# Optimization experiments

Hardware: AMD Instinct MI355X
Metric: run time of the kernel (lower is better)

Reference implementation:

```python
import jax, jax.numpy as jnp
import numpy as np
import math

DIM = 768
HEADS = 8
DIM_HEAD = 64
INNER = HEADS * DIM_HEAD  # 512
B, L = 2, 4096
LN_EPS = 1e-5


def setup_inputs() -> dict:
    key = jax.random.key(0)
    ks = jax.random.split(key, 6)
    std = 0.02
    return {
        "x": jax.random.normal(ks[0], (B, L, DIM), dtype=jnp.float32),
        "ln_gamma": jnp.ones((DIM,), dtype=jnp.float32),
        "ln_beta": jnp.zeros((DIM,), dtype=jnp.float32),
        "Wq": jax.random.normal(ks[1], (DIM, INNER), dtype=jnp.float32) * std,
        "Wkv": jax.random.normal(ks[2], (DIM, 2 * INNER), dtype=jnp.float32) * std,
        "Wo": jax.random.normal(ks[3], (INNER, DIM), dtype=jnp.float32) * std,
    }


def reference(x, ln_gamma, ln_beta, Wq, Wkv, Wo):
    b, l, _ = x.shape
    # LayerNorm (eps=1e-5, affine)
    mu = jnp.mean(x, axis=-1, keepdims=True)
    var = jnp.mean(jnp.square(x - mu), axis=-1, keepdims=True)
    xn = (x - mu) * jax.lax.rsqrt(var + LN_EPS) * ln_gamma + ln_beta

    q = xn @ Wq                      # (b, l, inner)
    kv = xn @ Wkv                    # (b, l, 2*inner)
    k, v = jnp.split(kv, 2, axis=-1)

    def to_heads(t):
        return t.reshape(b, l, HEADS, DIM_HEAD).transpose(0, 2, 1, 3)  # (b,h,l,d)

    q, k, v = to_heads(q), to_heads(k), to_heads(v)

    scale = 1.0 / math.sqrt(math.sqrt(DIM_HEAD))
    # explicit quadratic scores, softmax in float32 as in original
    weight = jnp.einsum("bhid,bhjd->bhij", q * scale, k * scale)
    weight = jax.nn.softmax(weight.astype(jnp.float32), axis=-1).astype(q.dtype)
    out = jnp.einsum("bhij,bhjd->bhid", weight, v)       # (b,h,l,d)
    out = out.transpose(0, 2, 1, 3).reshape(b, l, INNER)  # merge heads
    return out @ Wo
```

## Files before the change

kernel.cpp:

```cpp
#include <hip/hip_runtime.h>
#include <hip/hip_bf16.h>


typedef __bf16 bf16_t;
typedef __bf16 bf16x4 __attribute__((ext_vector_type(4)));
typedef __bf16 bf16x8 __attribute__((ext_vector_type(8)));
typedef float f32x4 __attribute__((ext_vector_type(4)));
typedef float f32x16 __attribute__((ext_vector_type(16)));
typedef unsigned int u32x2 __attribute__((ext_vector_type(2)));
typedef unsigned int u32x4 __attribute__((ext_vector_type(4)));

#define MFMA16(a, b, c) __builtin_amdgcn_mfma_f32_16x16x32_bf16((a), (b), (c), 0, 0, 0)
#define MFMA32(a, b, c) __builtin_amdgcn_mfma_f32_32x32x16_bf16((a), (b), (c), 0, 0, 0)

#define QSCALE 0.18033688011112042f

#define GLDS(gp, lp)                                                          \
    __builtin_amdgcn_global_load_lds(                                         \
        (const __attribute__((address_space(1))) void*)(gp),                  \
        (__attribute__((address_space(3))) void*)(lp), 16, 0, 0)

__device__ __forceinline__ int detect_f32(const unsigned int* __restrict__ xw) {
    const int l = threadIdx.x & 63;
    int cnt = 0;
#pragma unroll
    for (int j = 0; j < 2; ++j) {
        const unsigned int e = (xw[l * 2 + j] >> 7) & 0xFF;
        cnt += (e >= 100 && e <= 140) ? 1 : 0;
    }
#pragma unroll
    for (int off = 1; off < 64; off <<= 1) cnt += __shfl_xor(cnt, off, 64);
    return cnt < 64;
}

__global__ __launch_bounds__(256) void prep_kernel(
    const void* __restrict__ xv, const void* __restrict__ gv,
    const void* __restrict__ bv, const void* __restrict__ wq,
    const void* __restrict__ wkv, const void* __restrict__ wo,
    bf16_t* __restrict__ xn, bf16_t* __restrict__ WqkvT, bf16_t* __restrict__ WoT,
    int* __restrict__ flag) {
    const int f32 = detect_f32((const unsigned int*)xv);
    const int bid = blockIdx.x;
    const int t = threadIdx.x;
    if (bid == 0 && t == 0) *flag = f32;

    __shared__ bf16_t Ts[64 * 68];

    if (bid < 2048) {
        const int lane = t & 63;
        const int row = bid * 4 + (t >> 6);
        const int c0 = lane * 12;
        float v[12];
        if (f32) {
            const float* xr = (const float*)xv + (size_t)row * 768 + c0;
#pragma unroll
            for (int i = 0; i < 3; ++i) {
                const float4 q = *(const float4*)(xr + i * 4);
                v[i * 4] = q.x; v[i * 4 + 1] = q.y;
                v[i * 4 + 2] = q.z; v[i * 4 + 3] = q.w;
            }
        } else {
            const bf16_t* xr = (const bf16_t*)xv + (size_t)row * 768 + c0;
#pragma unroll
            for (int i = 0; i < 3; ++i) {
                const bf16x4 q = *(const bf16x4*)(xr + i * 4);
#pragma unroll
                for (int j = 0; j < 4; ++j) v[i * 4 + j] = (float)q[j];
            }
        }
        float s = 0.f, sq = 0.f;
#pragma unroll
        for (int j = 0; j < 12; ++j) { s += v[j]; sq += v[j] * v[j]; }
#pragma unroll
        for (int off = 1; off < 64; off <<= 1) {
            s += __shfl_xor(s, off, 64);
            sq += __shfl_xor(sq, off, 64);
        }
        const float mu = s * (1.0f / 768.0f);
        const float var = sq * (1.0f / 768.0f) - mu * mu;
        const float rstd = rsqrtf(var + 1e-5f);

        bf16_t* xo = xn + (size_t)row * 768 + c0;
#pragma unroll
        for (int i = 0; i < 3; ++i) {
            bf16x4 o;
#pragma unroll
            for (int j = 0; j < 4; ++j) {
                const int c = c0 + i * 4 + j;
                const float gc = f32 ? ((const float*)gv)[c] : (float)((const bf16_t*)gv)[c];
                const float bc = f32 ? ((const float*)bv)[c] : (float)((const bf16_t*)bv)[c];
                o[j] = (bf16_t)((v[i * 4 + j] - mu) * rstd * gc + bc);
            }
            *(bf16x4*)(xo + i * 4) = o;
        }
        return;
    }

    int idx = bid - 2048;
    const void* in;
    bf16_t* out;
    int R, C, cx, ry;
    if (idx < 96) {
        in = wq; out = WqkvT; R = 768; C = 512;
        cx = idx & 7; ry = idx >> 3;
    } else if (idx < 288) {
        idx -= 96;
        in = wkv; out = WqkvT + (size_t)512 * 768; R = 768; C = 1024;
        cx = idx & 15; ry = idx >> 4;
    } else {
        idx -= 288;
        in = wo; out = WoT; R = 512; C = 768;
        cx = idx % 12; ry = idx / 12;
    }
    const int r0 = ry * 64, c0 = cx * 64;
    {
        const int r = t >> 2, c = (t & 3) * 16;
        if (f32) {
            const float* src = (const float*)in + (size_t)(r0 + r) * C + c0 + c;
#pragma unroll
            for (int i = 0; i < 16; i += 4) {
                const float4 q = *(const float4*)(src + i);
                Ts[r * 68 + c + i] = (bf16_t)q.x;
                Ts[r * 68 + c + i + 1] = (bf16_t)q.y;
                Ts[r * 68 + c + i + 2] = (bf16_t)q.z;
                Ts[r * 68 + c + i + 3] = (bf16_t)q.w;
            }
        } else {
            const bf16_t* src = (const bf16_t*)in + (size_t)(r0 + r) * C + c0 + c;
            *(bf16x8*)&Ts[r * 68 + c] = *(const bf16x8*)src;
            *(bf16x8*)&Ts[r * 68 + c + 8] = *(const bf16x8*)(src + 8);
        }
    }
    __syncthreads();
    {
        const int oc = t >> 2, seg = (t & 3) * 16;
        bf16x8 v0, v1;
#pragma unroll
        for (int j = 0; j < 8; ++j) v0[j] = Ts[(seg + j) * 68 + oc];
#pragma unroll
        for (int j = 0; j < 8; ++j) v1[j] = Ts[(seg + 8 + j) * 68 + oc];
        bf16_t* dst = out + (size_t)(c0 + oc) * R + r0 + seg;
        *(bf16x8*)dst = v0;
        *(bf16x8*)(dst + 8) = v1;
    }
}

__global__ __launch_bounds__(256) void qkv_gemm(const bf16_t* __restrict__ A,
                                                const bf16_t* __restrict__ BT,
                                                bf16_t* __restrict__ qkv,
                                                bf16_t* __restrict__ vtg,
                                                int M, int N, int K) {
    const int m0 = blockIdx.y * 128;
    const int n0 = blockIdx.x * 128;
    __shared__ bf16_t As[128 * 32];
    __shared__ bf16_t Bs[128 * 32];

    const int t = threadIdx.x;
    const int lane = t & 63;
    const int w = t >> 6;
    const int wm = (w >> 1) * 64;
    const int wn = (w & 1) * 64;
    const int quad = lane >> 4;
    const int cl = lane & 15;

    f32x4 acc[4][4];
    const f32x4 z4 = {0.f, 0.f, 0.f, 0.f};
#pragma unroll
    for (int mi = 0; mi < 4; ++mi)
#pragma unroll
        for (int ni = 0; ni < 4; ++ni) acc[mi][ni] = z4;

    const int r0 = lane >> 2;
    const int c0 = (lane & 3) * 8;
    const bf16_t* AgL = A + (size_t)(m0 + w * 32 + r0) * K + c0;
    const bf16_t* AgH = A + (size_t)(m0 + w * 32 + 16 + r0) * K + c0;
    const bf16_t* BgL = BT + (size_t)(n0 + w * 32 + r0) * K + c0;
    const bf16_t* BgH = BT + (size_t)(n0 + w * 32 + 16 + r0) * K + c0;
    bf16_t* AdL = &As[(w * 32) * 32];
    bf16_t* AdH = &As[(w * 32 + 16) * 32];
    bf16_t* BdL = &Bs[(w * 32) * 32];
    bf16_t* BdH = &Bs[(w * 32 + 16) * 32];

    for (int kt = 0; kt < K; kt += 32) {
        __syncthreads();
        GLDS(AgL + kt, AdL);
        GLDS(AgH + kt, AdH);
        GLDS(BgL + kt, BdL);
        GLDS(BgH + kt, BdH);
        __syncthreads();

        const int ko = quad * 8;
        bf16x8 af[4], bfr[4];
#pragma unroll
        for (int mi = 0; mi < 4; ++mi)
            af[mi] = *(const bf16x8*)&As[(wm + mi * 16 + cl) * 32 + ko];
#pragma unroll
        for (int ni = 0; ni < 4; ++ni)
            bfr[ni] = *(const bf16x8*)&Bs[(wn + ni * 16 + cl) * 32 + ko];
#pragma unroll
        for (int mi = 0; mi < 4; ++mi)
#pragma unroll
            for (int ni = 0; ni < 4; ++ni)
                acc[mi][ni] = MFMA16(af[mi], bfr[ni], acc[mi][ni]);
    }

    if (n0 >= 1024) {
        const int b = m0 >> 12;
#pragma unroll
        for (int mi = 0; mi < 4; ++mi) {
#pragma unroll
            for (int ni = 0; ni < 4; ++ni) {
                const int tok = (m0 & 4095) + wm + mi * 16 + quad * 4;
                const int dl = n0 + wn + ni * 16 + cl - 1024;
                bf16x4 pk;
#pragma unroll
                for (int r4 = 0; r4 < 4; ++r4) pk[r4] = (bf16_t)acc[mi][ni][r4];
                *(bf16x4*)(vtg + ((size_t)(b * 8 + (dl >> 6)) * 64 + (dl & 63)) * 4096 +
                           tok) = pk;
            }
        }
    } else {
        const float sc = (n0 < 512) ? QSCALE : 1.0f;
#pragma unroll
        for (int mi = 0; mi < 4; ++mi) {
#pragma unroll
            for (int ni = 0; ni < 4; ++ni) {
#pragma unroll
                for (int r4 = 0; r4 < 4; ++r4) {
                    const int row = m0 + wm + mi * 16 + quad * 4 + r4;
                    const int col = n0 + wn + ni * 16 + cl;
                    qkv[(size_t)row * N + col] = (bf16_t)(acc[mi][ni][r4] * sc);
                }
            }
        }
    }
}

__global__ __launch_bounds__(128) void gemm_bt64(const bf16_t* __restrict__ A,
                                                 const bf16_t* __restrict__ BT,
                                                 void* __restrict__ C,
                                                 int M, int N, int K,
                                                 const int* __restrict__ out_flag) {
    const int m0 = blockIdx.y * 128;
    const int n0 = blockIdx.x * 64;
    __shared__ bf16_t As[128 * 32];
    __shared__ bf16_t Bs[64 * 32];

    const int t = threadIdx.x;
    const int lane = t & 63;
    const int w = t >> 6;
    const int quad = lane >> 4;
    const int cl = lane & 15;

    f32x4 acc[4][4];
    const f32x4 z4 = {0.f, 0.f, 0.f, 0.f};
#pragma unroll
    for (int mi = 0; mi < 4; ++mi)
#pragma unroll
        for (int ni = 0; ni < 4; ++ni) acc[mi][ni] = z4;

    const int r0 = lane >> 2;
    const int c0 = (lane & 3) * 8;
    const bf16_t* Ag = A + (size_t)(m0 + w * 64 + r0) * K + c0;
    const bf16_t* Bg = BT + (size_t)(n0 + w * 32 + r0) * K + c0;
    bf16_t* Ad = &As[(w * 64) * 32];
    bf16_t* Bd = &Bs[(w * 32) * 32];

    for (int kt = 0; kt < K; kt += 32) {
        __syncthreads();
#pragma unroll
        for (int i = 0; i < 4; ++i) GLDS(Ag + kt + (size_t)i * 16 * K, Ad + i * 512);
#pragma unroll
        for (int i = 0; i < 2; ++i) GLDS(Bg + kt + (size_t)i * 16 * K, Bd + i * 512);
        __syncthreads();

        const int ko = quad * 8;
        bf16x8 af[4], bfr[4];
#pragma unroll
        for (int mi = 0; mi < 4; ++mi)
            af[mi] = *(const bf16x8*)&As[(w * 64 + mi * 16 + cl) * 32 + ko];
#pragma unroll
        for (int ni = 0; ni < 4; ++ni)
            bfr[ni] = *(const bf16x8*)&Bs[(ni * 16 + cl) * 32 + ko];
#pragma unroll
        for (int mi = 0; mi < 4; ++mi)
#pragma unroll
            for (int ni = 0; ni < 4; ++ni)
                acc[mi][ni] = MFMA16(af[mi], bfr[ni], acc[mi][ni]);
    }

    const int f32out = *out_flag;
#pragma unroll
    for (int mi = 0; mi < 4; ++mi) {
#pragma unroll
        for (int ni = 0; ni < 4; ++ni) {
#pragma unroll
            for (int r4 = 0; r4 < 4; ++r4) {
                const int row = m0 + w * 64 + mi * 16 + quad * 4 + r4;
                const int col = n0 + ni * 16 + cl;
                if (f32out)
                    ((float*)C)[(size_t)row * N + col] = acc[mi][ni][r4];
                else
                    ((bf16_t*)C)[(size_t)row * N + col] = (bf16_t)acc[mi][ni][r4];
            }
        }
    }
}

__global__ __launch_bounds__(256, 2) void attn_kernel(const bf16_t* __restrict__ qkv,
                                                      const bf16_t* __restrict__ vtg,
                                                      bf16_t* __restrict__ ao) {
    const int qt = blockIdx.x;
    const int bh = blockIdx.y;
    const int b = bh >> 3, hd = bh & 7;

    __shared__ bf16_t Ks[2][64 * 64];
    __shared__ bf16_t Vs[2][64 * 64];

    const int t = threadIdx.x;
    const int lane = t & 63;
    const int w = t >> 6;
    const int c = lane & 31;
    const int h = lane >> 5;

    const size_t rowbase = (size_t)b * 4096;
    const int qcol = hd * 64;
    const int kcol = 512 + hd * 64;
    const int q0w = qt * 128 + w * 32;

    bf16x8 qf[4];
    {
        const bf16_t* qp = qkv + (rowbase + q0w + c) * 1536 + qcol + h * 8;
#pragma unroll
        for (int ks = 0; ks < 4; ++ks) qf[ks] = *(const bf16x8*)(qp + ks * 16);
    }

    bf16x8 ones;
#pragma unroll
    for (int e = 0; e < 8; ++e) ones[e] = (bf16_t)1.0f;

    f32x16 z16, o0, o1, l_acc;
#pragma unroll
    for (int i = 0; i < 16; ++i) z16[i] = 0.f;
    o0 = z16; o1 = z16; l_acc = z16;

    const int sr = t >> 3;
    const int seg = t & 7;
    const int swz = (seg ^ (sr & 7)) * 8;
    const bf16_t* kgp = qkv + (rowbase + sr) * 1536 + kcol + swz;
    const bf16_t* vgp = vtg + ((size_t)bh * 64 + sr) * 4096 + swz;

    int ksw[4];
#pragma unroll
    for (int ks = 0; ks < 4; ++ks) ksw[ks] = ((2 * ks + h) ^ (c & 7)) * 8;

    GLDS(kgp, &Ks[0][w * 512]);
    GLDS(kgp + (size_t)32 * 1536, &Ks[0][2048 + w * 512]);
    GLDS(vgp, &Vs[0][w * 512]);
    GLDS(vgp + (size_t)32 * 4096, &Vs[0][2048 + w * 512]);

    for (int it = 0; it < 64; ++it) {
        const int cur = it & 1;
        __syncthreads();

        if (it < 63) {
            const size_t gofs = (size_t)(it + 1) * 64;
            GLDS(kgp + gofs * 1536, &Ks[cur ^ 1][w * 512]);
            GLDS(kgp + (gofs + 32) * 1536, &Ks[cur ^ 1][2048 + w * 512]);
            GLDS(vgp + gofs, &Vs[cur ^ 1][w * 512]);
            GLDS(vgp + (size_t)32 * 4096 + gofs, &Vs[cur ^ 1][2048 + w * 512]);
        }

        __builtin_amdgcn_s_setprio(1);
        f32x16 s0, s1;
        {
            const bf16x8 k0 = *(const bf16x8*)&Ks[cur][c * 64 + ksw[0]];
            const bf16x8 k1 = *(const bf16x8*)&Ks[cur][(32 + c) * 64 + ksw[0]];
            s0 = MFMA32(k0, qf[0], z16);
            s1 = MFMA32(k1, qf[0], z16);
        }
#pragma unroll
        for (int ks = 1; ks < 4; ++ks) {
            const bf16x8 k0 = *(const bf16x8*)&Ks[cur][c * 64 + ksw[ks]];
            const bf16x8 k1 = *(const bf16x8*)&Ks[cur][(32 + c) * 64 + ksw[ks]];
            s0 = MFMA32(k0, qf[ks], s0);
            s1 = MFMA32(k1, qf[ks], s1);
        }
        __builtin_amdgcn_s_setprio(0);

        bf16x8 pf[4];
#pragma unroll
        for (int tt = 0; tt < 2; ++tt) {
            const f32x16 sv = tt ? s1 : s0;
            float ex[16];
#pragma unroll
            for (int i = 0; i < 16; ++i) ex[i] = exp2f(sv[i]);
            unsigned int pk[4][2];
#pragma unroll
            for (int g = 0; g < 4; ++g) {
                asm("v_cvt_pk_bf16_f32 %0, %1, %2"
                    : "=v"(pk[g][0]) : "v"(ex[4 * g + 0]), "v"(ex[4 * g + 1]));
                asm("v_cvt_pk_bf16_f32 %0, %1, %2"
                    : "=v"(pk[g][1]) : "v"(ex[4 * g + 2]), "v"(ex[4 * g + 3]));
            }
#pragma unroll
            for (int k2 = 0; k2 < 2; ++k2) {
                u32x4 fu;
#pragma unroll
                for (int cc = 0; cc < 2; ++cc) {
                    const u32x2 r = __builtin_amdgcn_permlane32_swap(
                        pk[2 * k2][cc], pk[2 * k2 + 1][cc], false, false);
                    fu[cc] = r[0];
                    fu[2 + cc] = r[1];
                }
                pf[tt * 2 + k2] = __builtin_bit_cast(bf16x8, fu);
            }
        }

        __builtin_amdgcn_s_setprio(1);
#pragma unroll
        for (int ks = 0; ks < 4; ++ks) {
            const bf16x8 v0 = *(const bf16x8*)&Vs[cur][c * 64 + ksw[ks]];
            const bf16x8 v1 = *(const bf16x8*)&Vs[cur][(32 + c) * 64 + ksw[ks]];
            o0 = MFMA32(pf[ks], v0, o0);
            o1 = MFMA32(pf[ks], v1, o1);
            l_acc = MFMA32(pf[ks], ones, l_acc);
        }
        __builtin_amdgcn_s_setprio(0);
    }

#pragma unroll
    for (int g = 0; g < 4; ++g) {
#pragma unroll
        for (int r4 = 0; r4 < 4; ++r4) {
            const int reg = 4 * g + r4;
            const int row = r4 + 8 * g + 4 * h;
            const float inv = 1.0f / l_acc[reg];
            bf16_t* op = ao + (rowbase + q0w + row) * 512 + qcol;
            op[c] = (bf16_t)(o0[reg] * inv);
            op[32 + c] = (bf16_t)(o1[reg] * inv);
        }
    }
}

extern "C" void kernel_launch(void* const* d_in, const int* in_sizes, int n_in,
                              void* d_out, int out_size, void* d_ws, size_t ws_size,
                              hipStream_t stream) {
    const void* x = d_in[0];
    const void* gamma = d_in[1];
    const void* beta = d_in[2];
    const void* Wq = d_in[3];
    const void* Wkv = d_in[4];
    const void* Wo = d_in[5];

    char* wsb = (char*)d_ws;
    int* flag = (int*)wsb;
    bf16_t* xn = (bf16_t*)(wsb + 256);
    bf16_t* WqkvT = xn + (size_t)8192 * 768;
    bf16_t* WoT = WqkvT + (size_t)1536 * 768;
    bf16_t* qkv = WoT + (size_t)768 * 512;
    bf16_t* aob = xn;
    bf16_t* vtg = (bf16_t*)d_out;

    prep_kernel<<<2432, 256, 0, stream>>>(x, gamma, beta, Wq, Wkv, Wo, xn, WqkvT, WoT,
                                          flag);

    qkv_gemm<<<dim3(12, 64), 256, 0, stream>>>(xn, WqkvT, qkv, vtg, 8192, 1536, 768);

    attn_kernel<<<dim3(32, 16), 256, 0, stream>>>(qkv, vtg, aob);

    gemm_bt64<<<dim3(12, 64), 128, 0, stream>>>(aob, WoT, d_out, 8192, 768, 512, flag);
}
```

Before: 266.0 us.

## Replace async global-to-LDS loads with register-staged padded LDS double buffering

The attention loop now loads K and V tiles into registers with ordinary global loads and stores them to LDS with a padded row stride of 68. This replaces the direct global_load_lds path and the XOR swizzle. The loop is unrolled by two, with fixed buffer pointers, and the exp is switched to the raw hardware exp2 builtin. The goal is to overlap global latency with compute through register prefetch and to simplify LDS addressing. The cost is higher register pressure and extra LDS store instructions.

Measured after the change: 381.8 us. 1.44x slower.

```diff
diff --git a/kernel.cpp b/kernel.cpp
--- a/kernel.cpp
+++ b/kernel.cpp
@@ -307,6 +307,69 @@
     }
 }
 
+__device__ __forceinline__ void attn_tile(const bf16_t* __restrict__ kb,
+                                          const bf16_t* __restrict__ vb,
+                                          const bf16x8* qf, const bf16x8 ones,
+                                          const f32x16 z16, f32x16& o0,
+                                          f32x16& o1, f32x16& l_acc) {
+    __builtin_amdgcn_s_setprio(1);
+    f32x16 s0, s1;
+    {
+        const bf16x8 k0 = *(const bf16x8*)(kb);
+        const bf16x8 k1 = *(const bf16x8*)(kb + 32 * 68);
+        s0 = MFMA32(k0, qf[0], z16);
+        s1 = MFMA32(k1, qf[0], z16);
+    }
+#pragma unroll
+    for (int ks = 1; ks < 4; ++ks) {
+        const bf16x8 k0 = *(const bf16x8*)(kb + ks * 16);
+        const bf16x8 k1 = *(const bf16x8*)(kb + 32 * 68 + ks * 16);
+        s0 = MFMA32(k0, qf[ks], s0);
+        s1 = MFMA32(k1, qf[ks], s1);
+    }
+    __builtin_amdgcn_s_setprio(0);
+
+    bf16x8 pf[4];
+#pragma unroll
+    for (int tt = 0; tt < 2; ++tt) {
+        const f32x16 sv = tt ? s1 : s0;
+        float ex[16];
+#pragma unroll
+        for (int i = 0; i < 16; ++i) ex[i] = __builtin_amdgcn_exp2f(sv[i]);
+        unsigned int pk[4][2];
+#pragma unroll
+        for (int g = 0; g < 4; ++g) {
+            asm("v_cvt_pk_bf16_f32 %0, %1, %2"
+                : "=v"(pk[g][0]) : "v"(ex[4 * g + 0]), "v"(ex[4 * g + 1]));
+            asm("v_cvt_pk_bf16_f32 %0, %1, %2"
+                : "=v"(pk[g][1]) : "v"(ex[4 * g + 2]), "v"(ex[4 * g + 3]));
+        }
+#pragma unroll
+        for (int k2 = 0; k2 < 2; ++k2) {
+            u32x4 fu;
+#pragma unroll
+            for (int cc = 0; cc < 2; ++cc) {
+                const u32x2 r = __builtin_amdgcn_permlane32_swap(
+                    pk[2 * k2][cc], pk[2 * k2 + 1][cc], false, false);
+                fu[cc] = r[0];
+                fu[2 + cc] = r[1];
+            }
+            pf[tt * 2 + k2] = __builtin_bit_cast(bf16x8, fu);
+        }
+    }
+
+    __builtin_amdgcn_s_setprio(1);
+#pragma unroll
+    for (int ks = 0; ks < 4; ++ks) {
+        const bf16x8 v0 = *(const bf16x8*)(vb + ks * 16);
+        const bf16x8 v1 = *(const bf16x8*)(vb + 32 * 68 + ks * 16);
+        o0 = MFMA32(pf[ks], v0, o0);
+        o1 = MFMA32(pf[ks], v1, o1);
+        l_acc = MFMA32(pf[ks], ones, l_acc);
+    }
+    __builtin_amdgcn_s_setprio(0);
+}
+
 __global__ __launch_bounds__(256, 2) void attn_kernel(const bf16_t* __restrict__ qkv,
                                                       const bf16_t* __restrict__ vtg,
                                                       bf16_t* __restrict__ ao) {
@@ -314,8 +377,8 @@
     const int bh = blockIdx.y;
     const int b = bh >> 3, hd = bh & 7;
 
-    __shared__ bf16_t Ks[2][64 * 64];
-    __shared__ bf16_t Vs[2][64 * 64];
+    __shared__ bf16_t Ks[2][64 * 68];
+    __shared__ bf16_t Vs[2][64 * 68];
 
     const int t = threadIdx.x;
     const int lane = t & 63;
@@ -346,88 +409,52 @@
 
     const int sr = t >> 3;
     const int seg = t & 7;
-    const int swz = (seg ^ (sr & 7)) * 8;
-    const bf16_t* kgp = qkv + (rowbase + sr) * 1536 + kcol + swz;
-    const bf16_t* vgp = vtg + ((size_t)bh * 64 + sr) * 4096 + swz;
-
-    int ksw[4];
-#pragma unroll
-    for (int ks = 0; ks < 4; ++ks) ksw[ks] = ((2 * ks + h) ^ (c & 7)) * 8;
-
-    GLDS(kgp, &Ks[0][w * 512]);
-    GLDS(kgp + (size_t)32 * 1536, &Ks[0][2048 + w * 512]);
-    GLDS(vgp, &Vs[0][w * 512]);
-    GLDS(vgp + (size_t)32 * 4096, &Vs[0][2048 + w * 512]);
-
-    for (int it = 0; it < 64; ++it) {
-        const int cur = it & 1;
+    const bf16_t* kgp = qkv + (rowbase + sr) * 1536 + kcol + seg * 8;
+    const bf16_t* vgp = vtg + ((size_t)bh * 64 + sr) * 4096 + seg * 8;
+
+    const bf16_t* kb0 = &Ks[0][c * 68 + h * 8];
+    const bf16_t* kb1 = &Ks[1][c * 68 + h * 8];
+    const bf16_t* vb0 = &Vs[0][c * 68 + h * 8];
+    const bf16_t* vb1 = &Vs[1][c * 68 + h * 8];
+
+    bf16x8 kA, kB, vA, vB;
+    int koff = 0, voff = 0;
+#define LOADN()                                                   \
+    do {                                                          \
+        kA = *(const bf16x8*)(kgp + koff);                        \
+        kB = *(const bf16x8*)(kgp + koff + 32 * 1536);            \
+        vA = *(const bf16x8*)(vgp + voff);                        \
+        vB = *(const bf16x8*)(vgp + voff + 32 * 4096);            \
+        koff += 64 * 1536;                                        \
+        voff += 64;                                               \
+    } while (0)
+#define STORE(b_)                                                 \
+    do {                                                          \
+        *(bf16x8*)&Ks[b_][sr * 68 + seg * 8] = kA;                \
+        *(bf16x8*)&Ks[b_][(sr + 32) * 68 + seg * 8] = kB;         \
+        *(bf16x8*)&Vs[b_][sr * 68 + seg * 8] = vA;                \
+        *(bf16x8*)&Vs[b_][(sr + 32) * 68 + seg * 8] = vB;         \
+    } while (0)
+
+    LOADN();
+    STORE(0);
+    LOADN();
+
+    for (int it2 = 0; it2 < 32; ++it2) {
         __syncthreads();
-
-        if (it < 63) {
-            const size_t gofs = (size_t)(it + 1) * 64;
-            GLDS(kgp + gofs * 1536, &Ks[cur ^ 1][w * 512]);
-            GLDS(kgp + (gofs + 32) * 1536, &Ks[cur ^ 1][2048 + w * 512]);
-            GLDS(vgp + gofs, &Vs[cur ^ 1][w * 512]);
-            GLDS(vgp + (size_t)32 * 4096 + gofs, &Vs[cur ^ 1][2048 + w * 512]);
-        }
-
-        __builtin_amdgcn_s_setprio(1);
-        f32x16 s0, s1;
-        {
-            const bf16x8 k0 = *(const bf16x8*)&Ks[cur][c * 64 + ksw[0]];
-            const bf16x8 k1 = *(const bf16x8*)&Ks[cur][(32 + c) * 64 + ksw[0]];
-            s0 = MFMA32(k0, qf[0], z16);
-            s1 = MFMA32(k1, qf[0], z16);
-        }
-#pragma unroll
-        for (int ks = 1; ks < 4; ++ks) {
-            const bf16x8 k0 = *(const bf16x8*)&Ks[cur][c * 64 + ksw[ks]];
-            const bf16x8 k1 = *(const bf16x8*)&Ks[cur][(32 + c) * 64 + ksw[ks]];
-            s0 = MFMA32(k0, qf[ks], s0);
-            s1 = MFMA32(k1, qf[ks], s1);
-        }
-        __builtin_amdgcn_s_setprio(0);
-
-        bf16x8 pf[4];
-#pragma unroll
-        for (int tt = 0; tt < 2; ++tt) {
-            const f32x16 sv = tt ? s1 : s0;
-            float ex[16];
-#pragma unroll
-            for (int i = 0; i < 16; ++i) ex[i] = exp2f(sv[i]);
-            unsigned int pk[4][2];
-#pragma unroll
-            for (int g = 0; g < 4; ++g) {
-                asm("v_cvt_pk_bf16_f32 %0, %1, %2"
-                    : "=v"(pk[g][0]) : "v"(ex[4 * g + 0]), "v"(ex[4 * g + 1]));
-                asm("v_cvt_pk_bf16_f32 %0, %1, %2"
-                    : "=v"(pk[g][1]) : "v"(ex[4 * g + 2]), "v"(ex[4 * g + 3]));
-            }
-#pragma unroll
-            for (int k2 = 0; k2 < 2; ++k2) {
-                u32x4 fu;
-#pragma unroll
-                for (int cc = 0; cc < 2; ++cc) {
-                    const u32x2 r = __builtin_amdgcn_permlane32_swap(
-                        pk[2 * k2][cc], pk[2 * k2 + 1][cc], false, false);
-                    fu[cc] = r[0];
-                    fu[2 + cc] = r[1];
-                }
-                pf[tt * 2 + k2] = __builtin_bit_cast(bf16x8, fu);
-            }
-        }
-
-        __builtin_amdgcn_s_setprio(1);
-#pragma unroll
-        for (int ks = 0; ks < 4; ++ks) {
-            const bf16x8 v0 = *(const bf16x8*)&Vs[cur][c * 64 + ksw[ks]];
-            const bf16x8 v1 = *(const bf16x8*)&Vs[cur][(32 + c) * 64 + ksw[ks]];
-            o0 = MFMA32(pf[ks], v0, o0);
-            o1 = MFMA32(pf[ks], v1, o1);
-            l_acc = MFMA32(pf[ks], ones, l_acc);
-        }
-        __builtin_amdgcn_s_setprio(0);
-    }
+        STORE(1);
+        if (it2 < 31) LOADN();
+        attn_tile(kb0, vb0, qf, ones, z16, o0, o1, l_acc);
+
+        __syncthreads();
+        if (it2 < 31) {
+            STORE(0);
+            LOADN();
+        }
+        attn_tile(kb1, vb1, qf, ones, z16, o0, o1, l_acc);
+    }
+#undef LOADN
+#undef STORE
 
 #pragma unroll
     for (int g = 0; g < 4; ++g) {
```

## Load K/V tiles directly from global into registers and remap attention grid

Applied to the files above, without the earlier changes.

The attention kernel drops the double-buffered LDS staging of K and V and the per-iteration barrier. Each wave now loads its K and V fragments straight from global memory into registers, prefetching the next K tile during softmax. The grid becomes 1D and is remapped so that blocks sharing a batch-head land on the same XCD for L2 reuse, and exp2f is replaced by the raw hardware exp2 builtin. The cost is that each of the four waves fetches K/V separately, which raises global/L2 traffic and register pressure and exposes load latency that LDS used to hide.

New measurement: 375.3 us. +41.1%, slower.

```diff
diff --git a/kernel.cpp b/kernel.cpp
--- a/kernel.cpp
+++ b/kernel.cpp
@@ -310,12 +310,11 @@
 __global__ __launch_bounds__(256, 2) void attn_kernel(const bf16_t* __restrict__ qkv,
                                                       const bf16_t* __restrict__ vtg,
                                                       bf16_t* __restrict__ ao) {
-    const int qt = blockIdx.x;
-    const int bh = blockIdx.y;
+    const int bid = blockIdx.x;
+    const int i = bid >> 3;
+    const int bh = (bid & 7) * 2 + (i >> 5);
+    const int qt = i & 31;
     const int b = bh >> 3, hd = bh & 7;
-
-    __shared__ bf16_t Ks[2][64 * 64];
-    __shared__ bf16_t Vs[2][64 * 64];
 
     const int t = threadIdx.x;
     const int lane = t & 63;
@@ -341,52 +340,48 @@
 
     f32x16 z16, o0, o1, l_acc;
 #pragma unroll
-    for (int i = 0; i < 16; ++i) z16[i] = 0.f;
+    for (int i2 = 0; i2 < 16; ++i2) z16[i2] = 0.f;
     o0 = z16; o1 = z16; l_acc = z16;
 
-    const int sr = t >> 3;
-    const int seg = t & 7;
-    const int swz = (seg ^ (sr & 7)) * 8;
-    const bf16_t* kgp = qkv + (rowbase + sr) * 1536 + kcol + swz;
-    const bf16_t* vgp = vtg + ((size_t)bh * 64 + sr) * 4096 + swz;
-
-    int ksw[4];
-#pragma unroll
-    for (int ks = 0; ks < 4; ++ks) ksw[ks] = ((2 * ks + h) ^ (c & 7)) * 8;
-
-    GLDS(kgp, &Ks[0][w * 512]);
-    GLDS(kgp + (size_t)32 * 1536, &Ks[0][2048 + w * 512]);
-    GLDS(vgp, &Vs[0][w * 512]);
-    GLDS(vgp + (size_t)32 * 4096, &Vs[0][2048 + w * 512]);
+    const bf16_t* kp0 = qkv + (rowbase + c) * 1536 + kcol + h * 8;
+    const bf16_t* kp1 = kp0 + (size_t)32 * 1536;
+    const bf16_t* vp0 = vtg + ((size_t)bh * 64 + c) * 4096 + h * 8;
+    const bf16_t* vp1 = vp0 + (size_t)32 * 4096;
+
+    bf16x8 kc[8];
+#pragma unroll
+    for (int ks = 0; ks < 4; ++ks) {
+        kc[ks] = *(const bf16x8*)(kp0 + ks * 16);
+        kc[4 + ks] = *(const bf16x8*)(kp1 + ks * 16);
+    }
 
     for (int it = 0; it < 64; ++it) {
-        const int cur = it & 1;
-        __syncthreads();
+        bf16x8 vc[8];
+#pragma unroll
+        for (int ks = 0; ks < 4; ++ks) {
+            vc[ks] = *(const bf16x8*)(vp0 + ks * 16);
+            vc[4 + ks] = *(const bf16x8*)(vp1 + ks * 16);
+        }
+        vp0 += 64; vp1 += 64;
+
+        __builtin_amdgcn_s_setprio(1);
+        f32x16 s0 = MFMA32(kc[0], qf[0], z16);
+        f32x16 s1 = MFMA32(kc[4], qf[0], z16);
+#pragma unroll
+        for (int ks = 1; ks < 4; ++ks) {
+            s0 = MFMA32(kc[ks], qf[ks], s0);
+            s1 = MFMA32(kc[4 + ks], qf[ks], s1);
+        }
+        __builtin_amdgcn_s_setprio(0);
 
         if (it < 63) {
-            const size_t gofs = (size_t)(it + 1) * 64;
-            GLDS(kgp + gofs * 1536, &Ks[cur ^ 1][w * 512]);
-            GLDS(kgp + (gofs + 32) * 1536, &Ks[cur ^ 1][2048 + w * 512]);
-            GLDS(vgp + gofs, &Vs[cur ^ 1][w * 512]);
-            GLDS(vgp + (size_t)32 * 4096 + gofs, &Vs[cur ^ 1][2048 + w * 512]);
-        }
-
-        __builtin_amdgcn_s_setprio(1);
-        f32x16 s0, s1;
-        {
-            const bf16x8 k0 = *(const bf16x8*)&Ks[cur][c * 64 + ksw[0]];
-            const bf16x8 k1 = *(const bf16x8*)&Ks[cur][(32 + c) * 64 + ksw[0]];
-            s0 = MFMA32(k0, qf[0], z16);
-            s1 = MFMA32(k1, qf[0], z16);
-        }
-#pragma unroll
-        for (int ks = 1; ks < 4; ++ks) {
-            const bf16x8 k0 = *(const bf16x8*)&Ks[cur][c * 64 + ksw[ks]];
-            const bf16x8 k1 = *(const bf16x8*)&Ks[cur][(32 + c) * 64 + ksw[ks]];
-            s0 = MFMA32(k0, qf[ks], s0);
-            s1 = MFMA32(k1, qf[ks], s1);
-        }
-        __builtin_amdgcn_s_setprio(0);
+            kp0 += (size_t)64 * 1536; kp1 += (size_t)64 * 1536;
+#pragma unroll
+            for (int ks = 0; ks < 4; ++ks) {
+                kc[ks] = *(const bf16x8*)(kp0 + ks * 16);
+                kc[4 + ks] = *(const bf16x8*)(kp1 + ks * 16);
+            }
+        }
 
         bf16x8 pf[4];
 #pragma unroll
@@ -394,7 +389,7 @@
             const f32x16 sv = tt ? s1 : s0;
             float ex[16];
 #pragma unroll
-            for (int i = 0; i < 16; ++i) ex[i] = exp2f(sv[i]);
+            for (int i3 = 0; i3 < 16; ++i3) ex[i3] = __builtin_amdgcn_exp2f(sv[i3]);
             unsigned int pk[4][2];
 #pragma unroll
             for (int g = 0; g < 4; ++g) {
@@ -420,10 +415,8 @@
         __builtin_amdgcn_s_setprio(1);
 #pragma unroll
         for (int ks = 0; ks < 4; ++ks) {
-            const bf16x8 v0 = *(const bf16x8*)&Vs[cur][c * 64 + ksw[ks]];
-            const bf16x8 v1 = *(const bf16x8*)&Vs[cur][(32 + c) * 64 + ksw[ks]];
-            o0 = MFMA32(pf[ks], v0, o0);
-            o1 = MFMA32(pf[ks], v1, o1);
+            o0 = MFMA32(pf[ks], vc[ks], o0);
+            o1 = MFMA32(pf[ks], vc[4 + ks], o1);
             l_acc = MFMA32(pf[ks], ones, l_acc);
         }
         __builtin_amdgcn_s_setprio(0);
@@ -467,7 +460,7 @@
 
     qkv_gemm<<<dim3(12, 64), 256, 0, stream>>>(xn, WqkvT, qkv, vtg, 8192, 1536, 768);
 
-    attn_kernel<<<dim3(32, 16), 256, 0, stream>>>(qkv, vtg, aob);
+    attn_kernel<<<512, 256, 0, stream>>>(qkv, vtg, aob);
 
     gemm_bt64<<<dim3(12, 64), 128, 0, stream>>>(aob, WoT, d_out, 8192, 768, 512, flag);
 }
```
